# Performance work log

Hardware: AMD Instinct MI355X
Metric: run time of the kernel (lower is better)

Reference implementation:

```python
import jax, jax.numpy as jnp
import numpy as np
from jax import lax

T, N, C, H, W = 16, 8, 64, 64, 64  # out_channels=64, in_channels=2*C
DAMPENING = 0.9
SUPPORT = 1.0

@jax.custom_vjp
def spike(x):
    return (x > 0).astype(x.dtype)

def _spike_fwd(x):
    return spike(x), x

def _spike_bwd(x, g):
    # pseudo-derivative: dampening * max(0, 1 - |x|/support)
    return (DAMPENING * jnp.maximum(0.0, 1.0 - jnp.abs(x) / SUPPORT) * g,)

spike.defvjp(_spike_fwd, _spike_bwd)

def _conv(x, w, b):
    # NCHW x OIHW -> NCHW, 3x3, pad 1, stride 1
    y = lax.conv_general_dilated(x, w, window_strides=(1, 1),
                                 padding=((1, 1), (1, 1)),
                                 dimension_numbers=('NCHW', 'OIHW', 'NCHW'))
    return y + b[None, :, None, None]

def setup_inputs() -> dict:
    key = jax.random.key(0)
    ks = jax.random.split(key, 6)
    fan = C * 3 * 3
    scale = 1.0 / np.sqrt(fan)
    xt = jax.random.normal(ks[0], (T, N, 2 * C, H, W), dtype=jnp.float32)
    w_rz = jax.random.normal(ks[1], (C, C, 3, 3), dtype=jnp.float32) * scale
    b_rz = jax.random.normal(ks[2], (C,), dtype=jnp.float32) * scale
    w_f = jax.random.normal(ks[3], (C, C, 3, 3), dtype=jnp.float32) * scale
    b_f = jax.random.normal(ks[4], (C,), dtype=jnp.float32) * scale
    thr_reparam = jax.random.normal(ks[5], (H, W), dtype=jnp.float32) * np.sqrt(2.0)
    return {"xt": xt, "w_rz": w_rz, "b_rz": b_rz, "w_f": w_f, "b_f": b_f,
            "thr_reparam": thr_reparam, "stage": 0}

def reference(xt, w_rz, b_rz, w_f, b_f, thr_reparam, stage):
    thr = jax.nn.sigmoid(thr_reparam)  # [H, W], broadcasts over [N, C, H, W]
    prev_y0 = jnp.zeros((N, C, H, W), dtype=xt.dtype)
    h0 = jnp.zeros((N, C, H, W), dtype=xt.dtype)

    def step(carry, xi):
        prev_y, h = carry
        xi_i, xi_f = jnp.split(xi, 2, axis=1)
        forget_gate = jax.nn.sigmoid(_conv(prev_y, w_rz, b_rz) + xi_i)
        input_gate = jnp.tanh(_conv(prev_y * forget_gate, w_f, b_f) + xi_f)
        h = (1.0 - forget_gate) * h + forget_gate * input_gate
        d = h - thr
        event = spike(d)
        neg_dist = jnp.where(d < 0, thr - h, 0.0)
        y = h * event
        h_next = h - event * thr
        return (y, h_next), (y, event, neg_dist)

    _, (ys, events, neg_dists) = lax.scan(step, (prev_y0, h0), xt)
    return ys, events, neg_dists
```

## Files before the change

### kernel.cpp

```cpp
#include <hip/hip_runtime.h>
#include <cstdint>

typedef _Float16 half8 __attribute__((ext_vector_type(8)));
typedef _Float16 half4 __attribute__((ext_vector_type(4)));
typedef float f32x4 __attribute__((ext_vector_type(4)));

#define T_STEPS 16
#define NB 8
#define CCH 64
#define HH 64
#define WW 64
#define HW 4096
#define NCHW (NB * CCH * HW)
#define XTSTR (NB * 2 * CCH * HW)

#define CI_PAD 40
#define IN_LDS (4 * 66 * CI_PAD)

__device__ __forceinline__ void split2h(float x, _Float16& hi, _Float16& lo) {
    hi = (_Float16)x;
    lo = (_Float16)((x - (float)hi) * 2048.0f);
}

__global__ __launch_bounds__(256) void prep_w(const float* __restrict__ w_rz,
                                              const float* __restrict__ w_f,
                                              _Float16* __restrict__ w_hi,
                                              _Float16* __restrict__ w_lo) {
    int i = blockIdx.x * 256 + threadIdx.x;
    if (i >= 2 * 9 * 2 * 2 * 32 * 32) return;
    int ci = i & 31, co = (i >> 5) & 31, ch = (i >> 10) & 1, chunk = (i >> 11) & 1;
    int gt = i >> 12; int tap = gt % 9; int g = gt / 9;
    const float* w = g ? w_f : w_rz;
    float v = w[(size_t)((ch * 32 + co) * CCH + (chunk * 32 + ci)) * 9 + tap];
    _Float16 hi, lo; split2h(v, hi, lo);
    w_hi[i] = hi; w_lo[i] = lo;
}

__device__ __forceinline__ void stage_pl(const _Float16* __restrict__ ph,
                                         const _Float16* __restrict__ pl,
                                         int n, int y0, int chunk,
                                         _Float16* __restrict__ s_hi,
                                         _Float16* __restrict__ s_lo, int tid) {
    #pragma unroll
    for (int it = 0; it < 5; ++it) {
        int i = tid + it * 256;
        if (i >= 1056) break;
        int gg = i & 3; int tmp = i >> 2; int c = tmp % 66; int r = tmp / 66;
        int gr = y0 - 1 + r, gc = c - 1;
        uint4 uh = make_uint4(0, 0, 0, 0), ul = make_uint4(0, 0, 0, 0);
        if ((unsigned)gr < 64u && (unsigned)gc < 64u) {
            size_t base = (((size_t)n * 64 + gr) * 64 + gc) * 64 + chunk * 32 + gg * 8;
            uh = *(const uint4*)(ph + base);
            ul = *(const uint4*)(pl + base);
        }
        int off = (r * 66 + c) * CI_PAD + gg * 8;
        *(uint4*)&s_hi[off] = uh;
        *(uint4*)&s_lo[off] = ul;
    }
}

__device__ __forceinline__ void wloadp(const _Float16* __restrict__ wh,
                                       const _Float16* __restrict__ wl,
                                       int fg, int ch, int tid, uint2* uh, uint2* ul) {
    int chunk = fg / 3, ty = fg - chunk * 3;
    #pragma unroll
    for (int tx = 0; tx < 3; ++tx) {
        size_t base = (size_t)(((ty * 3 + tx) * 2 + chunk) * 2 + ch) * 1024 + tid * 4;
        uh[tx] = *(const uint2*)(wh + base);
        ul[tx] = *(const uint2*)(wl + base);
    }
}
__device__ __forceinline__ void wwritep(const uint2* uh, const uint2* ul,
                                        _Float16 (*sw)[2][1024], int tid) {
    int co = tid >> 3, j = tid & 7;
    int pos = ((j >> 1) ^ (co ^ (co >> 2))) & 3;
    int off = co * 32 + pos * 8 + (j & 1) * 4;
    #pragma unroll
    for (int tx = 0; tx < 3; ++tx) {
        *(uint2*)&sw[tx][0][off] = uh[tx];
        *(uint2*)&sw[tx][1][off] = ul[tx];
    }
}

__device__ __forceinline__ void conv_core(const _Float16* __restrict__ in_h,
    const _Float16* __restrict__ in_l, const _Float16* __restrict__ wh,
    const _Float16* __restrict__ wl, int n, int y0, int ch, int tid,
    f32x4 acc1[2][2], f32x4 acc2[2][2],
    _Float16* s_in_h, _Float16* s_in_l, _Float16 (*s_w)[3][2][1024]) {

    int wv = tid >> 6, l = tid & 63, lg = l >> 4, ln = l & 15;
    int aoff = ln * 32 + ((lg ^ ln ^ (ln >> 2)) & 3) * 8;

    uint2 wrh[3], wrl[3];
    stage_pl(in_h, in_l, n, y0, 0, s_in_h, s_in_l, tid);
    wloadp(wh, wl, 0, ch, tid, wrh, wrl);
    wwritep(wrh, wrl, s_w[0], tid);
    wloadp(wh, wl, 1, ch, tid, wrh, wrl);
    __syncthreads();

    int db = 0;
    for (int gi = 0; gi < 6; ++gi) {
        int ty = gi % 3;
        if (gi < 5) {
            wwritep(wrh, wrl, s_w[db ^ 1], tid);
            if (gi + 2 < 6) wloadp(wh, wl, gi + 2, ch, tid, wrh, wrl);
        }
        #pragma unroll
        for (int tx = 0; tx < 3; ++tx) {
            half8 afh[2], afl[2];
            #pragma unroll
            for (int ct = 0; ct < 2; ++ct) {
                afh[ct] = *(const half8*)&s_w[db][tx][0][ct * 512 + aoff];
                afl[ct] = *(const half8*)&s_w[db][tx][1][ct * 512 + aoff];
            }
            half8 bfh[2], bfl[2];
            #pragma unroll
            for (int st = 0; st < 2; ++st) {
                int sp = wv * 32 + st * 16 + ln;
                int boff = (((sp >> 6) + ty) * 66 + (sp & 63) + tx) * CI_PAD + lg * 8;
                bfh[st] = *(const half8*)&s_in_h[boff];
                bfl[st] = *(const half8*)&s_in_l[boff];
            }
            #pragma unroll
            for (int ct = 0; ct < 2; ++ct)
                #pragma unroll
                for (int st = 0; st < 2; ++st) {
                    acc1[ct][st] = __builtin_amdgcn_mfma_f32_16x16x32_f16(afh[ct], bfh[st], acc1[ct][st], 0, 0, 0);
                    acc2[ct][st] = __builtin_amdgcn_mfma_f32_16x16x32_f16(afh[ct], bfl[st], acc2[ct][st], 0, 0, 0);
                    acc2[ct][st] = __builtin_amdgcn_mfma_f32_16x16x32_f16(afl[ct], bfh[st], acc2[ct][st], 0, 0, 0);
                }
        }
        if (gi == 2) {
            __syncthreads();
            stage_pl(in_h, in_l, n, y0, 1, s_in_h, s_in_l, tid);
        }
        __syncthreads();
        db ^= 1;
    }
}

template<bool ZERO>
__global__ __launch_bounds__(256, 2) void kA(
    const _Float16* __restrict__ y_hi, const _Float16* __restrict__ y_lo,
    const _Float16* __restrict__ wh, const _Float16* __restrict__ wl,
    const float* __restrict__ b_rz, const float* __restrict__ xt_t,
    float* __restrict__ f_out,
    _Float16* __restrict__ a_hi, _Float16* __restrict__ a_lo) {

    __shared__ __align__(16) _Float16 s_in_h[IN_LDS];
    __shared__ __align__(16) _Float16 s_in_l[IN_LDS];
    __shared__ __align__(16) _Float16 s_w[2][3][2][1024];

    int tid = threadIdx.x, wv = tid >> 6, l = tid & 63, lg = l >> 4, ln = l & 15;
    int bid = ((blockIdx.x & 7) << 6) | (blockIdx.x >> 3);
    int n = bid >> 6, strip = (bid >> 1) & 31, ch = bid & 1, y0 = strip * 2;

    float xi_r[2][2][4];
    half4 pyh_r[2][2], pyl_r[2][2];
    float brz_[2][4];
    #pragma unroll
    for (int ct = 0; ct < 2; ++ct) {
        #pragma unroll
        for (int st = 0; st < 2; ++st) {
            int sp = wv * 32 + st * 16 + ln, row = y0 + (sp >> 6), col = sp & 63;
            size_t pb = (((size_t)n * 64 + row) * 64 + col) * 64
                      + ch * 32 + ct * 16 + lg * 4;
            if (!ZERO) {
                pyh_r[ct][st] = *(const half4*)(y_hi + pb);
                pyl_r[ct][st] = *(const half4*)(y_lo + pb);
            } else {
                pyh_r[ct][st] = half4{}; pyl_r[ct][st] = half4{};
            }
            #pragma unroll
            for (int r = 0; r < 4; ++r) {
                int co = ch * 32 + ct * 16 + lg * 4 + r;
                xi_r[ct][st][r] = xt_t[((n * 2 * CCH + co) * HH + row) * WW + col];
            }
        }
        #pragma unroll
        for (int r = 0; r < 4; ++r)
            brz_[ct][r] = b_rz[ch * 32 + ct * 16 + lg * 4 + r];
    }

    f32x4 acc1[2][2] = {}, acc2[2][2] = {};
    if (!ZERO)
        conv_core(y_hi, y_lo, wh, wl, n, y0, ch, tid, acc1, acc2, s_in_h, s_in_l, s_w);

    #pragma unroll
    for (int ct = 0; ct < 2; ++ct)
        #pragma unroll
        for (int st = 0; st < 2; ++st) {
            int sp = wv * 32 + st * 16 + ln, row = y0 + (sp >> 6), col = sp & 63;
            size_t pb = (((size_t)n * 64 + row) * 64 + col) * 64 + ch * 32 + ct * 16 + lg * 4;
            half4 avh, avl;
            #pragma unroll
            for (int r = 0; r < 4; ++r) {
                int co = ch * 32 + ct * 16 + lg * 4 + r;
                float conv = ZERO ? 0.0f
                    : (acc1[ct][st][r] + acc2[ct][st][r] * (1.0f / 2048.0f));
                int idx = ((n * CCH + co) * HH + row) * WW + col;
                float s = conv + brz_[ct][r] + xi_r[ct][st][r];
                float f = 1.0f / (1.0f + expf(-s));
                f_out[idx] = f;
                float py = (float)pyh_r[ct][st][r] + (float)pyl_r[ct][st][r] * (1.0f / 2048.0f);
                float a = py * f;
                _Float16 hi, lo; split2h(a, hi, lo);
                avh[r] = hi; avl[r] = lo;
            }
            if (!ZERO) {
                *(half4*)(a_hi + pb) = avh;
                *(half4*)(a_lo + pb) = avl;
            }
        }
}

template<bool ZERO>
__global__ __launch_bounds__(256, 2) void kB(
    const _Float16* __restrict__ a_hi, const _Float16* __restrict__ a_lo,
    const _Float16* __restrict__ wh, const _Float16* __restrict__ wl,
    const float* __restrict__ b_f, const float* __restrict__ xt_t,
    const float* __restrict__ f_in, const float* __restrict__ thr_rp,
    float* __restrict__ h_buf, float* __restrict__ ys,
    float* __restrict__ ev, float* __restrict__ nd,
    _Float16* __restrict__ y_hi, _Float16* __restrict__ y_lo) {

    __shared__ __align__(16) _Float16 s_in_h[IN_LDS];
    __shared__ __align__(16) _Float16 s_in_l[IN_LDS];
    __shared__ __align__(16) _Float16 s_w[2][3][2][1024];

    int tid = threadIdx.x, wv = tid >> 6, l = tid & 63, lg = l >> 4, ln = l & 15;
    int bid = ((blockIdx.x & 7) << 6) | (blockIdx.x >> 3);
    int n = bid >> 6, strip = (bid >> 1) & 31, ch = bid & 1, y0 = strip * 2;

    float xi_r[2][2][4], f_r[2][2][4], h_r[2][2][4];
    float thr_r[2], bf_[2][4];
    #pragma unroll
    for (int st = 0; st < 2; ++st) {
        int sp = wv * 32 + st * 16 + ln, row = y0 + (sp >> 6), col = sp & 63;
        thr_r[st] = thr_rp[row * WW + col];
    }
    #pragma unroll
    for (int ct = 0; ct < 2; ++ct) {
        #pragma unroll
        for (int st = 0; st < 2; ++st) {
            int sp = wv * 32 + st * 16 + ln, row = y0 + (sp >> 6), col = sp & 63;
            #pragma unroll
            for (int r = 0; r < 4; ++r) {
                int co = ch * 32 + ct * 16 + lg * 4 + r;
                int idx = ((n * CCH + co) * HH + row) * WW + col;
                xi_r[ct][st][r] = xt_t[((n * 2 * CCH + CCH + co) * HH + row) * WW + col];
                f_r[ct][st][r]  = f_in[idx];
                h_r[ct][st][r]  = ZERO ? 0.0f : h_buf[idx];
            }
        }
        #pragma unroll
        for (int r = 0; r < 4; ++r)
            bf_[ct][r] = b_f[ch * 32 + ct * 16 + lg * 4 + r];
    }

    f32x4 acc1[2][2] = {}, acc2[2][2] = {};
    if (!ZERO)
        conv_core(a_hi, a_lo, wh, wl, n, y0, ch, tid, acc1, acc2, s_in_h, s_in_l, s_w);

    #pragma unroll
    for (int ct = 0; ct < 2; ++ct)
        #pragma unroll
        for (int st = 0; st < 2; ++st) {
            int sp = wv * 32 + st * 16 + ln, row = y0 + (sp >> 6), col = sp & 63;
            float thr = 1.0f / (1.0f + expf(-thr_r[st]));
            size_t pb = (((size_t)n * 64 + row) * 64 + col) * 64 + ch * 32 + ct * 16 + lg * 4;
            half4 yvh, yvl;
            #pragma unroll
            for (int r = 0; r < 4; ++r) {
                int co = ch * 32 + ct * 16 + lg * 4 + r;
                float conv = ZERO ? 0.0f
                    : (acc1[ct][st][r] + acc2[ct][st][r] * (1.0f / 2048.0f));
                int idx = ((n * CCH + co) * HH + row) * WW + col;
                float s  = conv + bf_[ct][r] + xi_r[ct][st][r];
                float e2 = expf(2.0f * s);
                float g  = 1.0f - 2.0f / (e2 + 1.0f);
                float f  = f_r[ct][st][r];
                float hp = h_r[ct][st][r];
                float h  = (1.0f - f) * hp + f * g;
                float d  = h - thr;
                bool  e  = d > 0.0f;
                float y  = e ? h : 0.0f;
                ys[idx] = y;
                ev[idx] = e ? 1.0f : 0.0f;
                nd[idx] = (d < 0.0f) ? (thr - h) : 0.0f;
                h_buf[idx] = e ? d : h;
                _Float16 hi, lo; split2h(y, hi, lo);
                yvh[r] = hi; yvl[r] = lo;
            }
            *(half4*)(y_hi + pb) = yvh;
            *(half4*)(y_lo + pb) = yvl;
        }
}

extern "C" void kernel_launch(void* const* d_in, const int* in_sizes, int n_in,
                              void* d_out, int out_size, void* d_ws, size_t ws_size,
                              hipStream_t stream) {
    (void)in_sizes; (void)n_in; (void)out_size; (void)ws_size;

    const float* xt     = (const float*)d_in[0];
    const float* w_rz   = (const float*)d_in[1];
    const float* b_rz   = (const float*)d_in[2];
    const float* w_f    = (const float*)d_in[3];
    const float* b_f    = (const float*)d_in[4];
    const float* thr_rp = (const float*)d_in[5];

    float* out = (float*)d_out;
    _Float16* y_hi = (_Float16*)d_ws;
    _Float16* y_lo = y_hi + NCHW;
    _Float16* a_hi = y_lo + NCHW;
    _Float16* a_lo = a_hi + NCHW;
    float*    f_buf = (float*)(a_lo + NCHW);
    float*    h_buf = f_buf + NCHW;
    _Float16* w_hi  = (_Float16*)(h_buf + NCHW);
    _Float16* w_lo  = w_hi + 73728;

    float* ys0 = out;
    float* ev0 = out + (size_t)T_STEPS * NCHW;
    float* nd0 = ev0 + (size_t)T_STEPS * NCHW;

    prep_w<<<288, 256, 0, stream>>>(w_rz, w_f, w_hi, w_lo);
    const _Float16* whA = w_hi,         * wlA = w_lo;
    const _Float16* whB = w_hi + 36864, * wlB = w_lo + 36864;

    dim3 grid(512), block(256);
    for (int t = 0; t < T_STEPS; ++t) {
        const float* xt_t = xt + (size_t)t * XTSTR;
        float* ys_t = ys0 + (size_t)t * NCHW;
        float* ev_t = ev0 + (size_t)t * NCHW;
        float* nd_t = nd0 + (size_t)t * NCHW;
        if (t == 0) {
            kA<true><<<grid, block, 0, stream>>>(y_hi, y_lo, whA, wlA, b_rz, xt_t,
                                                 f_buf, a_hi, a_lo);
            kB<true><<<grid, block, 0, stream>>>(a_hi, a_lo, whB, wlB, b_f, xt_t,
                                                 f_buf, thr_rp, h_buf,
                                                 ys_t, ev_t, nd_t, y_hi, y_lo);
        } else {
            kA<false><<<grid, block, 0, stream>>>(y_hi, y_lo, whA, wlA, b_rz, xt_t,
                                                  f_buf, a_hi, a_lo);
            kB<false><<<grid, block, 0, stream>>>(a_hi, a_lo, whB, wlB, b_f, xt_t,
                                                  f_buf, thr_rp, h_buf,
                                                  ys_t, ev_t, nd_t, y_hi, y_lo);
        }
    }
}
```

Baseline: 672.4 us.

## Stage all nine weight taps per chunk and prefetch next chunk into registers

Replaces the per-row double-buffered weight pipeline, which had six groups each followed by a barrier, with a two-phase scheme. All nine taps of one input-channel chunk are staged in LDS, and the second chunk's input tile and weights are loaded into registers while the first chunk's MFMAs run. This reduces barriers from about seven to three per conv. The cost is higher register pressure from 18 uint2 plus 10 uint4 prefetch registers and LDS that grows from 24KB to 36KB for weights, which may hurt occupancy at launch_bounds(256,2).

```diff
diff --git a/kernel.cpp b/kernel.cpp
--- a/kernel.cpp
+++ b/kernel.cpp
@@ -59,26 +59,92 @@
     }
 }
 
-__device__ __forceinline__ void wloadp(const _Float16* __restrict__ wh,
+__device__ __forceinline__ void stage_issue2(const _Float16* __restrict__ ph,
+                                             const _Float16* __restrict__ pl,
+                                             int n, int y0, int chunk, int tid,
+                                             uint4* vh, uint4* vl) {
+    #pragma unroll
+    for (int it = 0; it < 5; ++it) {
+        int i = tid + it * 256;
+        vh[it] = make_uint4(0, 0, 0, 0);
+        vl[it] = make_uint4(0, 0, 0, 0);
+        if (i < 1056) {
+            int gg = i & 3; int tmp = i >> 2; int c = tmp % 66; int r = tmp / 66;
+            int gr = y0 - 1 + r, gc = c - 1;
+            if ((unsigned)gr < 64u && (unsigned)gc < 64u) {
+                size_t base = (((size_t)n * 64 + gr) * 64 + gc) * 64 + chunk * 32 + gg * 8;
+                vh[it] = *(const uint4*)(ph + base);
+                vl[it] = *(const uint4*)(pl + base);
+            }
+        }
+    }
+}
+__device__ __forceinline__ void stage_write2(const uint4* vh, const uint4* vl,
+                                             _Float16* __restrict__ s_hi,
+                                             _Float16* __restrict__ s_lo, int tid) {
+    #pragma unroll
+    for (int it = 0; it < 5; ++it) {
+        int i = tid + it * 256;
+        if (i < 1056) {
+            int gg = i & 3, cell = i >> 2;
+            int off = cell * CI_PAD + gg * 8;
+            *(uint4*)&s_hi[off] = vh[it];
+            *(uint4*)&s_lo[off] = vl[it];
+        }
+    }
+}
+
+__device__ __forceinline__ void wload9(const _Float16* __restrict__ wh,
                                        const _Float16* __restrict__ wl,
-                                       int fg, int ch, int tid, uint2* uh, uint2* ul) {
-    int chunk = fg / 3, ty = fg - chunk * 3;
-    #pragma unroll
-    for (int tx = 0; tx < 3; ++tx) {
-        size_t base = (size_t)(((ty * 3 + tx) * 2 + chunk) * 2 + ch) * 1024 + tid * 4;
-        uh[tx] = *(const uint2*)(wh + base);
-        ul[tx] = *(const uint2*)(wl + base);
-    }
-}
-__device__ __forceinline__ void wwritep(const uint2* uh, const uint2* ul,
+                                       int chunk, int ch, int tid,
+                                       uint2* uh, uint2* ul) {
+    #pragma unroll
+    for (int tap = 0; tap < 9; ++tap) {
+        size_t base = (size_t)((tap * 2 + chunk) * 2 + ch) * 1024 + tid * 4;
+        uh[tap] = *(const uint2*)(wh + base);
+        ul[tap] = *(const uint2*)(wl + base);
+    }
+}
+__device__ __forceinline__ void wwrite9(const uint2* uh, const uint2* ul,
                                         _Float16 (*sw)[2][1024], int tid) {
     int co = tid >> 3, j = tid & 7;
     int pos = ((j >> 1) ^ (co ^ (co >> 2))) & 3;
     int off = co * 32 + pos * 8 + (j & 1) * 4;
     #pragma unroll
-    for (int tx = 0; tx < 3; ++tx) {
-        *(uint2*)&sw[tx][0][off] = uh[tx];
-        *(uint2*)&sw[tx][1][off] = ul[tx];
+    for (int tap = 0; tap < 9; ++tap) {
+        *(uint2*)&sw[tap][0][off] = uh[tap];
+        *(uint2*)&sw[tap][1][off] = ul[tap];
+    }
+}
+
+__device__ __forceinline__ void chunk_mfma(const _Float16* __restrict__ s_in_h,
+    const _Float16* __restrict__ s_in_l, _Float16 (*s_w)[2][1024],
+    int wv, int lg, int ln, int aoff, f32x4 acc1[2][2], f32x4 acc2[2][2]) {
+    #pragma unroll
+    for (int tap = 0; tap < 9; ++tap) {
+        const int ty = tap / 3, tx = tap - ty * 3;
+        half8 afh[2], afl[2];
+        #pragma unroll
+        for (int ct = 0; ct < 2; ++ct) {
+            afh[ct] = *(const half8*)&s_w[tap][0][ct * 512 + aoff];
+            afl[ct] = *(const half8*)&s_w[tap][1][ct * 512 + aoff];
+        }
+        half8 bfh[2], bfl[2];
+        #pragma unroll
+        for (int st = 0; st < 2; ++st) {
+            int sp = wv * 32 + st * 16 + ln;
+            int boff = (((sp >> 6) + ty) * 66 + (sp & 63) + tx) * CI_PAD + lg * 8;
+            bfh[st] = *(const half8*)&s_in_h[boff];
+            bfl[st] = *(const half8*)&s_in_l[boff];
+        }
+        #pragma unroll
+        for (int ct = 0; ct < 2; ++ct)
+            #pragma unroll
+            for (int st = 0; st < 2; ++st) {
+                acc1[ct][st] = __builtin_amdgcn_mfma_f32_16x16x32_f16(afh[ct], bfh[st], acc1[ct][st], 0, 0, 0);
+                acc2[ct][st] = __builtin_amdgcn_mfma_f32_16x16x32_f16(afh[ct], bfl[st], acc2[ct][st], 0, 0, 0);
+                acc2[ct][st] = __builtin_amdgcn_mfma_f32_16x16x32_f16(afl[ct], bfh[st], acc2[ct][st], 0, 0, 0);
+            }
     }
 }
 
@@ -86,57 +152,32 @@
     const _Float16* __restrict__ in_l, const _Float16* __restrict__ wh,
     const _Float16* __restrict__ wl, int n, int y0, int ch, int tid,
     f32x4 acc1[2][2], f32x4 acc2[2][2],
-    _Float16* s_in_h, _Float16* s_in_l, _Float16 (*s_w)[3][2][1024]) {
+    _Float16* s_in_h, _Float16* s_in_l, _Float16 (*s_w)[2][1024]) {
 
     int wv = tid >> 6, l = tid & 63, lg = l >> 4, ln = l & 15;
     int aoff = ln * 32 + ((lg ^ ln ^ (ln >> 2)) & 3) * 8;
 
-    uint2 wrh[3], wrl[3];
     stage_pl(in_h, in_l, n, y0, 0, s_in_h, s_in_l, tid);
-    wloadp(wh, wl, 0, ch, tid, wrh, wrl);
-    wwritep(wrh, wrl, s_w[0], tid);
-    wloadp(wh, wl, 1, ch, tid, wrh, wrl);
+    {
+        uint2 w0h[9], w0l[9];
+        wload9(wh, wl, 0, ch, tid, w0h, w0l);
+        wwrite9(w0h, w0l, s_w, tid);
+    }
     __syncthreads();
 
-    int db = 0;
-    for (int gi = 0; gi < 6; ++gi) {
-        int ty = gi % 3;
-        if (gi < 5) {
-            wwritep(wrh, wrl, s_w[db ^ 1], tid);
-            if (gi + 2 < 6) wloadp(wh, wl, gi + 2, ch, tid, wrh, wrl);
-        }
-        #pragma unroll
-        for (int tx = 0; tx < 3; ++tx) {
-            half8 afh[2], afl[2];
-            #pragma unroll
-            for (int ct = 0; ct < 2; ++ct) {
-                afh[ct] = *(const half8*)&s_w[db][tx][0][ct * 512 + aoff];
-                afl[ct] = *(const half8*)&s_w[db][tx][1][ct * 512 + aoff];
-            }
-            half8 bfh[2], bfl[2];
-            #pragma unroll
-            for (int st = 0; st < 2; ++st) {
-                int sp = wv * 32 + st * 16 + ln;
-                int boff = (((sp >> 6) + ty) * 66 + (sp & 63) + tx) * CI_PAD + lg * 8;
-                bfh[st] = *(const half8*)&s_in_h[boff];
-                bfl[st] = *(const half8*)&s_in_l[boff];
-            }
-            #pragma unroll
-            for (int ct = 0; ct < 2; ++ct)
-                #pragma unroll
-                for (int st = 0; st < 2; ++st) {
-                    acc1[ct][st] = __builtin_amdgcn_mfma_f32_16x16x32_f16(afh[ct], bfh[st], acc1[ct][st], 0, 0, 0);
-                    acc2[ct][st] = __builtin_amdgcn_mfma_f32_16x16x32_f16(afh[ct], bfl[st], acc2[ct][st], 0, 0, 0);
-                    acc2[ct][st] = __builtin_amdgcn_mfma_f32_16x16x32_f16(afl[ct], bfh[st], acc2[ct][st], 0, 0, 0);
-                }
-        }
-        if (gi == 2) {
-            __syncthreads();
-            stage_pl(in_h, in_l, n, y0, 1, s_in_h, s_in_l, tid);
-        }
-        __syncthreads();
-        db ^= 1;
-    }
+    uint4 sh1[5], sl1[5];
+    uint2 w1h[9], w1l[9];
+    stage_issue2(in_h, in_l, n, y0, 1, tid, sh1, sl1);
+    wload9(wh, wl, 1, ch, tid, w1h, w1l);
+
+    chunk_mfma(s_in_h, s_in_l, s_w, wv, lg, ln, aoff, acc1, acc2);
+
+    __syncthreads();
+    stage_write2(sh1, sl1, s_in_h, s_in_l, tid);
+    wwrite9(w1h, w1l, s_w, tid);
+    __syncthreads();
+
+    chunk_mfma(s_in_h, s_in_l, s_w, wv, lg, ln, aoff, acc1, acc2);
 }
 
 template<bool ZERO>
@@ -149,7 +190,7 @@
 
     __shared__ __align__(16) _Float16 s_in_h[IN_LDS];
     __shared__ __align__(16) _Float16 s_in_l[IN_LDS];
-    __shared__ __align__(16) _Float16 s_w[2][3][2][1024];
+    __shared__ __align__(16) _Float16 s_w[9][2][1024];
 
     int tid = threadIdx.x, wv = tid >> 6, l = tid & 63, lg = l >> 4, ln = l & 15;
     int bid = ((blockIdx.x & 7) << 6) | (blockIdx.x >> 3);
@@ -226,7 +267,7 @@
 
     __shared__ __align__(16) _Float16 s_in_h[IN_LDS];
     __shared__ __align__(16) _Float16 s_in_l[IN_LDS];
-    __shared__ __align__(16) _Float16 s_w[2][3][2][1024];
+    __shared__ __align__(16) _Float16 s_w[9][2][1024];
 
     int tid = threadIdx.x, wv = tid >> 6, l = tid & 63, lg = l >> 4, ln = l & 15;
     int bid = ((blockIdx.x & 7) << 6) | (blockIdx.x >> 3);
```

New measurement: 608.7 us. 9.5% less time.
